# Performance work log

Measured on AMD Instinct MI355X. Metric: run time of the kernel, lower is better.

## Reference

```python
import jax, jax.numpy as jnp
import numpy as np

B, S, D = 4, 1024, 1024
NS = 8            # n_samples
NT = 10           # n_steps
EXP_NOISE = 0.1
STEP = 0.01
TEMP = 1.0
LN_EPS = 1e-5


def _ln(x, g, b):
    m = jnp.mean(x, axis=-1, keepdims=True)
    v = jnp.mean(jnp.square(x - m), axis=-1, keepdims=True)
    return (x - m) * jax.lax.rsqrt(v + LN_EPS) * g + b


def setup_inputs() -> dict:
    key = jax.random.key(0)
    ks = jax.random.split(key, 8)
    sc = 0.02
    return {
        "hidden": jax.random.normal(ks[0], (B, S, D), jnp.float32),
        "W1": jax.random.normal(ks[1], (D, 2 * D), jnp.float32) * sc,
        "b1": jnp.zeros((2 * D,), jnp.float32),
        "ln1_g": jnp.ones((2 * D,), jnp.float32),
        "ln1_b": jnp.zeros((2 * D,), jnp.float32),
        "W2": jax.random.normal(ks[2], (2 * D, D), jnp.float32) * sc,
        "b2": jnp.zeros((D,), jnp.float32),
        "Ew1": jax.random.normal(ks[3], (2 * D, D), jnp.float32) * sc,
        "Eb1": jnp.zeros((D,), jnp.float32),
        "Eln_g": jnp.ones((D,), jnp.float32),
        "Eln_b": jnp.zeros((D,), jnp.float32),
        "Ew2": jax.random.normal(ks[4], (D, D // 2), jnp.float32) * sc,
        "Eb2": jnp.zeros((D // 2,), jnp.float32),
        "Ew3": jax.random.normal(ks[5], (D // 2, 1), jnp.float32) * sc,
        "Eb3": jnp.zeros((1,), jnp.float32),
    }


def reference(hidden, W1, b1, ln1_g, ln1_b, W2, b2,
              Ew1, Eb1, Eln_g, Eln_b, Ew2, Eb2, Ew3, Eb3):
    # context: per-seq mean, identical at every position (keepdim+expand in torch)
    ctx = jnp.mean(hidden, axis=1)                      # [B, D]
    # context_predictor (result is .detach()-ed inside pcn_refine)
    cp = jax.nn.relu(_ln(ctx @ W1 + b1, ln1_g, ln1_b)) @ W2 + b2   # [B, D]
    cp = jax.lax.stop_gradient(cp)

    nkey = jax.random.key(42)
    # n_samples exploration hypotheses: hidden + N(0, exploration_noise)
    expl = jax.random.normal(jax.random.fold_in(nkey, 0), (NS, B, S, D), hidden.dtype)
    hyp = hidden[None] + expl * EXP_NOISE               # [NS, B, S, D]

    cpb = cp[None, :, None, :]                          # broadcast to [NS,B,S,D]

    # PCN refinement: linear pull toward cp + small noise on all but last step
    def step_fn(cur, t):
        cur = cur - STEP * (cur - cpb)
        noise = jax.random.normal(jax.random.fold_in(nkey, t + 1), cur.shape, cur.dtype)
        cur = cur + noise * 0.01 * (t < NT - 1)
        return cur, None

    hyp, _ = jax.lax.scan(step_fn, hyp, jnp.arange(NT))

    # energy_net on concat([latent, context]): split first linear to avoid concat
    Ew1_h, Ew1_c = Ew1[:D], Ew1[D:]
    ce = ctx @ Ew1_c + Eb1                              # context contribution [B, D]
    e = hyp @ Ew1_h + ce[None, :, None, :]              # [NS, B, S, D]
    e = jax.nn.relu(_ln(e, Eln_g, Eln_b))
    e = jax.nn.relu(e @ Ew2 + Eb2)                      # [NS, B, S, D//2]
    e = (e @ Ew3 + Eb3)[..., 0]                         # [NS, B, S]
    energies = jnp.mean(e, axis=2)                      # [NS, B]

    probs = jax.nn.softmax(-energies / TEMP, axis=0)    # [NS, B]
    selected = jnp.einsum('nb,nbsd->bsd', probs, hyp)   # [B, S, D]
    return selected
```

## Files before the change

### kernel.cpp

```cpp
#include <hip/hip_runtime.h>
#include <hip/hip_bf16.h>
#include <stdint.h>
#include <math.h>


#define NS_ 8
#define B_ 4
#define S_ 1024
#define D_ 1024
#define NROWS (NS_*B_*S_)
#define NELEM (1u<<25)

typedef __attribute__((ext_vector_type(8))) short short8;
typedef __attribute__((ext_vector_type(4))) float f32x4;

struct RngParams {
  uint32_t k0[10], k1[10];
  float coef[10];
  float aH, aCP;
};

__host__ __device__ __forceinline__ uint32_t rotl32_(uint32_t x, int r) {
  return (x << r) | (x >> (32 - r));
}

__host__ __device__ __forceinline__ void tf2x32(uint32_t k0, uint32_t k1,
                                                uint32_t x0, uint32_t x1,
                                                uint32_t &o0, uint32_t &o1) {
  uint32_t k2 = k0 ^ k1 ^ 0x1BD11BDAu;
  x0 += k0; x1 += k1;
  x0 += x1; x1 = rotl32_(x1, 13); x1 ^= x0;
  x0 += x1; x1 = rotl32_(x1, 15); x1 ^= x0;
  x0 += x1; x1 = rotl32_(x1, 26); x1 ^= x0;
  x0 += x1; x1 = rotl32_(x1, 6);  x1 ^= x0;
  x0 += k1; x1 += k2 + 1u;
  x0 += x1; x1 = rotl32_(x1, 17); x1 ^= x0;
  x0 += x1; x1 = rotl32_(x1, 29); x1 ^= x0;
  x0 += x1; x1 = rotl32_(x1, 16); x1 ^= x0;
  x0 += x1; x1 = rotl32_(x1, 24); x1 ^= x0;
  x0 += k2; x1 += k0 + 2u;
  x0 += x1; x1 = rotl32_(x1, 13); x1 ^= x0;
  x0 += x1; x1 = rotl32_(x1, 15); x1 ^= x0;
  x0 += x1; x1 = rotl32_(x1, 26); x1 ^= x0;
  x0 += x1; x1 = rotl32_(x1, 6);  x1 ^= x0;
  x0 += k0; x1 += k1 + 3u;
  x0 += x1; x1 = rotl32_(x1, 17); x1 ^= x0;
  x0 += x1; x1 = rotl32_(x1, 29); x1 ^= x0;
  x0 += x1; x1 = rotl32_(x1, 16); x1 ^= x0;
  x0 += x1; x1 = rotl32_(x1, 24); x1 ^= x0;
  x0 += k1; x1 += k2 + 4u;
  x0 += x1; x1 = rotl32_(x1, 13); x1 ^= x0;
  x0 += x1; x1 = rotl32_(x1, 15); x1 ^= x0;
  x0 += x1; x1 = rotl32_(x1, 26); x1 ^= x0;
  x0 += x1; x1 = rotl32_(x1, 6);  x1 ^= x0;
  x0 += k2; x1 += k0 + 5u;
  o0 = x0; o1 = x1;
}

__device__ __forceinline__ float bits_to_normal(uint32_t bits) {
  const float lo = -0.99999994f;
  float f = __uint_as_float((bits >> 9) | 0x3f800000u) - 1.0f;
  float x = fmaxf(lo, f * 2.0f + lo);
  float t = (1.0f - x) * (1.0f + x);
  float w = -__logf(t);
  float p;
  if (w < 5.0f) {
    w = w - 2.5f;
    p = 2.81022636e-08f;
    p = fmaf(p, w, 3.43273939e-07f);
    p = fmaf(p, w, -3.5233877e-06f);
    p = fmaf(p, w, -4.39150654e-06f);
    p = fmaf(p, w, 0.00021858087f);
    p = fmaf(p, w, -0.00125372503f);
    p = fmaf(p, w, -0.00417768164f);
    p = fmaf(p, w, 0.246640727f);
    p = fmaf(p, w, 1.50140941f);
  } else {
    w = sqrtf(w) - 3.0f;
    p = -0.000200214257f;
    p = fmaf(p, w, 0.000100950558f);
    p = fmaf(p, w, 0.00134934322f);
    p = fmaf(p, w, -0.00367342844f);
    p = fmaf(p, w, 0.00573950773f);
    p = fmaf(p, w, -0.0076224613f);
    p = fmaf(p, w, 0.00943887047f);
    p = fmaf(p, w, 1.00167406f);
    p = fmaf(p, w, 2.83297682f);
  }
  return 1.41421356f * (p * x);
}

__device__ __forceinline__ float noise10(const RngParams& P, uint32_t i) {
  float acc = 0.f;
  #pragma unroll
  for (int j = 0; j < 10; ++j) {
    uint32_t w0, w1;
    tf2x32(P.k0[j], P.k1[j], 0u, i, w0, w1);
    acc = fmaf(P.coef[j], bits_to_normal(w0 ^ w1), acc);
  }
  return acc;
}

__device__ __forceinline__ uint16_t bf16u(float x) {
  __hip_bfloat16 h = __float2bfloat16(x);
  return *(uint16_t*)&h;
}
__device__ __forceinline__ float bf2f(uint32_t u) {
  return __uint_as_float(u << 16);
}

__global__ void k_ctxA(const float* __restrict__ hidden, float* __restrict__ part) {
  int b = blockIdx.x >> 6, ch = blockIdx.x & 63;
  const float* p = hidden + (size_t)b * (S_ * D_) + (size_t)ch * 16 * 1024;
  int tid = threadIdx.x;
  #pragma unroll
  for (int k = 0; k < 4; ++k) {
    int d = tid + k * 256;
    float s = 0.f;
    #pragma unroll
    for (int t = 0; t < 16; ++t) s += p[t * 1024 + d];
    part[(size_t)blockIdx.x * 1024 + d] = s;
  }
}
__global__ void k_ctxB(const float* __restrict__ part, float* __restrict__ ctx) {
  int idx = blockIdx.x * 256 + threadIdx.x;
  int b = idx >> 10, d = idx & 1023;
  float s = 0.f;
  #pragma unroll 8
  for (int c = 0; c < 64; ++c) s += part[((size_t)(b * 64 + c)) * 1024 + d];
  ctx[idx] = s * (1.0f / 1024.0f);
}

__global__ void k_fc1(const float* __restrict__ ctx, const float* __restrict__ W1,
                      const float* __restrict__ b1, float* __restrict__ t1) {
  __shared__ float red[4][64];
  int b = blockIdx.x >> 5;
  int j0 = (blockIdx.x & 31) * 64;
  int l = threadIdx.x & 63, w = threadIdx.x >> 6;
  int j = j0 + l;
  const float* c = ctx + b * 1024 + w * 256;
  const float* wp = W1 + (size_t)(w * 256) * 2048 + j;
  float s = 0.f;
  #pragma unroll 8
  for (int k = 0; k < 256; ++k) s += c[k] * wp[(size_t)k * 2048];
  red[w][l] = s; __syncthreads();
  if (w == 0)
    t1[b * 2048 + j] = red[0][l] + red[1][l] + red[2][l] + red[3][l] + b1[j];
}

__global__ void k_ln_relu(float* __restrict__ t1, const float* __restrict__ g,
                          const float* __restrict__ bb) {
  __shared__ float red[256];
  int row = blockIdx.x, tid = threadIdx.x;
  float* x = t1 + row * 2048;
  float v[8];
  #pragma unroll
  for (int q = 0; q < 8; ++q) v[q] = x[tid + q * 256];
  float s = 0.f;
  #pragma unroll
  for (int q = 0; q < 8; ++q) s += v[q];
  red[tid] = s; __syncthreads();
  for (int off = 128; off > 0; off >>= 1) { if (tid < off) red[tid] += red[tid + off]; __syncthreads(); }
  float m = red[0] * (1.0f / 2048.0f);
  __syncthreads();
  float s2 = 0.f;
  #pragma unroll
  for (int q = 0; q < 8; ++q) { float d = v[q] - m; s2 += d * d; }
  red[tid] = s2; __syncthreads();
  for (int off = 128; off > 0; off >>= 1) { if (tid < off) red[tid] += red[tid + off]; __syncthreads(); }
  float var = red[0] * (1.0f / 2048.0f);
  float rs = 1.0f / sqrtf(var + 1e-5f);
  #pragma unroll
  for (int q = 0; q < 8; ++q) {
    int j = tid + q * 256;
    float z = (v[q] - m) * rs * g[j] + bb[j];
    x[j] = fmaxf(z, 0.0f);
  }
}

__global__ void k_fc2(const float* __restrict__ t1, const float* __restrict__ W2,
                      const float* __restrict__ b2, const float* __restrict__ ctx,
                      const float* __restrict__ Ew1c, const float* __restrict__ Eb1,
                      float* __restrict__ cp, float* __restrict__ ce) {
  __shared__ float red[4][64];
  int b = blockIdx.x >> 4;
  int j0 = (blockIdx.x & 15) * 64;
  int l = threadIdx.x & 63, w = threadIdx.x >> 6;
  int j = j0 + l;
  float s = 0.f;
  if (blockIdx.y == 0) {
    const float* a = t1 + b * 2048 + w * 512;
    const float* wp = W2 + (size_t)(w * 512) * 1024 + j;
    #pragma unroll 8
    for (int k = 0; k < 512; ++k) s += a[k] * wp[(size_t)k * 1024];
  } else {
    const float* a = ctx + b * 1024 + w * 256;
    const float* wp = Ew1c + (size_t)(w * 256) * 1024 + j;
    #pragma unroll 8
    for (int k = 0; k < 256; ++k) s += a[k] * wp[(size_t)k * 1024];
  }
  red[w][l] = s; __syncthreads();
  if (w == 0) {
    float r = red[0][l] + red[1][l] + red[2][l] + red[3][l];
    if (blockIdx.y == 0) cp[b * 1024 + j] = r + b2[j];
    else                 ce[b * 1024 + j] = r + Eb1[j];
  }
}

__global__ void k_wcvt(const float* __restrict__ src, uint16_t* __restrict__ dst,
                       int K, int N) {
  __shared__ float tile[64][65];
  int n0 = blockIdx.x * 64, k0 = blockIdx.y * 64;
  int tid = threadIdx.x;
  #pragma unroll
  for (int i = 0; i < 16; ++i) {
    int lin = tid + i * 256;
    int tr = lin >> 6, tc = lin & 63;
    tile[tr][tc] = src[(size_t)(k0 + tr) * N + n0 + tc];
  }
  __syncthreads();
  #pragma unroll
  for (int i = 0; i < 8; ++i) {
    int lin = tid + i * 256;
    int tr = lin >> 5, tc2 = (lin & 31) * 2;
    uint32_t pk = (uint32_t)bf16u(tile[tc2][tr]) | ((uint32_t)bf16u(tile[tc2 + 1][tr]) << 16);
    *(uint32_t*)(&dst[(size_t)(n0 + tr) * K + k0 + tc2]) = pk;
  }
}

#define APAN 0
#define ZPAN 32768
#define BSOF 65536

__device__ __forceinline__ int pswz(int row, int byteInRow) {
  return (row * 2048 + byteInRow) ^ ((row & 7) << 4);
}
__device__ __forceinline__ int bswz(int c, int kbyte) {
  return (c * 64 + kbyte) ^ ((c & 7) << 4);
}

template<bool BIG>
__global__ __launch_bounds__(256, 2) void k_fused(
    const float* __restrict__ hidden, const float* __restrict__ cp,
    const float* __restrict__ ce, uint32_t* __restrict__ hypPairs,
    const uint16_t* __restrict__ WT1, const uint16_t* __restrict__ WT2,
    const float* __restrict__ Eln_g, const float* __restrict__ Eln_b,
    const float* __restrict__ Eb2, const float* __restrict__ Ew3,
    float* __restrict__ erows, RngParams P)
{
  __shared__ __align__(16) char smem[81920];
  const int tid = threadIdx.x;
  const int lane = tid & 63;
  const int w = tid >> 6;
  const int rl = lane & 15;
  const int kg = lane >> 4;
  const int r0 = blockIdx.x * 16;
  const int bidx = (r0 >> 10) & 3;

  for (int q = 0; q < 32; ++q) {
    int p = tid + q * 256;
    int row = p >> 9, cpi = p & 511;
    int c0 = cpi * 2;
    uint32_t i0 = (uint32_t)(r0 + row) * 1024u + (uint32_t)c0;
    float nz0 = noise10(P, i0);
    float nz1 = noise10(P, i0 + 1u);
    uint32_t bsd = i0 & 0x3FFFFFu;
    float2 hv = *(const float2*)(hidden + bsd);
    float2 cv = *(const float2*)(cp + (bidx << 10) + c0);
    float h0 = fmaf(P.aH, hv.x, fmaf(P.aCP, cv.x, nz0));
    float h1 = fmaf(P.aH, hv.y, fmaf(P.aCP, cv.y, nz1));
    uint32_t pk = (uint32_t)bf16u(h0) | ((uint32_t)bf16u(h1) << 16);
    *(uint32_t*)(smem + APAN + pswz(row, c0 * 2)) = pk;
    if (BIG) hypPairs[i0 >> 1] = pk;
  }
  __syncthreads();

  uint4 wreg0, wreg1, wreg2, wreg3;
  for (int g = 0; g < 4; ++g) {
    f32x4 acc[4] = {};
    {
      const uint16_t* srcb = WT1 + (size_t)(g * 256) * 1024;
      int f0 = tid, f1 = tid + 256, f2 = tid + 512, f3 = tid + 768;
      wreg0 = *(const uint4*)(srcb + (size_t)(f0 >> 2) * 1024 + (f0 & 3) * 8);
      wreg1 = *(const uint4*)(srcb + (size_t)(f1 >> 2) * 1024 + (f1 & 3) * 8);
      wreg2 = *(const uint4*)(srcb + (size_t)(f2 >> 2) * 1024 + (f2 & 3) * 8);
      wreg3 = *(const uint4*)(srcb + (size_t)(f3 >> 2) * 1024 + (f3 & 3) * 8);
    }
    for (int kt = 0; kt < 32; ++kt) {
      __syncthreads();
      {
        int f0 = tid, f1 = tid + 256, f2 = tid + 512, f3 = tid + 768;
        *(uint4*)(smem + BSOF + bswz(f0 >> 2, (f0 & 3) * 16)) = wreg0;
        *(uint4*)(smem + BSOF + bswz(f1 >> 2, (f1 & 3) * 16)) = wreg1;
        *(uint4*)(smem + BSOF + bswz(f2 >> 2, (f2 & 3) * 16)) = wreg2;
        *(uint4*)(smem + BSOF + bswz(f3 >> 2, (f3 & 3) * 16)) = wreg3;
      }
      if (kt < 31) {
        const uint16_t* srcb = WT1 + (size_t)(g * 256) * 1024 + (kt + 1) * 32;
        int f0 = tid, f1 = tid + 256, f2 = tid + 512, f3 = tid + 768;
        wreg0 = *(const uint4*)(srcb + (size_t)(f0 >> 2) * 1024 + (f0 & 3) * 8);
        wreg1 = *(const uint4*)(srcb + (size_t)(f1 >> 2) * 1024 + (f1 & 3) * 8);
        wreg2 = *(const uint4*)(srcb + (size_t)(f2 >> 2) * 1024 + (f2 & 3) * 8);
        wreg3 = *(const uint4*)(srcb + (size_t)(f3 >> 2) * 1024 + (f3 & 3) * 8);
      }
      __syncthreads();
      short8 af = *(const short8*)(smem + APAN + pswz(rl, kt * 64 + kg * 16));
      #pragma unroll
      for (int j = 0; j < 4; ++j) {
        int cl = w * 64 + j * 16 + rl;
        short8 bf = *(const short8*)(smem + BSOF + bswz(cl, kg * 16));
        acc[j] = __builtin_amdgcn_mfma_f32_16x16x32_bf16(af, bf, acc[j], 0, 0, 0);
      }
    }
    #pragma unroll
    for (int j = 0; j < 4; ++j) {
      int C = g * 256 + w * 64 + j * 16 + rl;
      float cev = ce[(bidx << 10) + C];
      #pragma unroll
      for (int i = 0; i < 4; ++i) {
        int row = kg * 4 + i;
        *(uint16_t*)(smem + ZPAN + pswz(row, C * 2)) = bf16u(acc[j][i] + cev);
      }
    }
  }
  __syncthreads();

  float* rowm = (float*)(smem + BSOF);
  float* rowr = rowm + 16;
  if (tid < 128) {
    int row = tid >> 3, l8 = tid & 7;
    float s1 = 0.f, s2 = 0.f;
    for (int j = 0; j < 128; ++j) {
      int c = l8 + j * 8;
      float v = bf2f(*(const uint16_t*)(smem + ZPAN + pswz(row, c * 2)));
      s1 += v; s2 = fmaf(v, v, s2);
    }
    #pragma unroll
    for (int o = 4; o > 0; o >>= 1) {
      s1 += __shfl_down(s1, o, 8);
      s2 += __shfl_down(s2, o, 8);
    }
    if (l8 == 0) {
      float m = s1 * (1.0f / 1024.0f);
      float var = fmaxf(s2 * (1.0f / 1024.0f) - m * m, 0.0f);
      rowm[row] = m;
      rowr[row] = 1.0f / sqrtf(var + 1e-5f);
    }
  }
  __syncthreads();

  for (int q = 0; q < 64; ++q) {
    int e = tid + q * 256;
    int row = e >> 10, col = e & 1023;
    uint16_t* zp = (uint16_t*)(smem + ZPAN + pswz(row, col * 2));
    float v = bf2f(*zp);
    float z = (v - rowm[row]) * rowr[row] * Eln_g[col] + Eln_b[col];
    *zp = bf16u(fmaxf(z, 0.f));
  }
  __syncthreads();

  float ep0 = 0.f, ep1 = 0.f, ep2 = 0.f, ep3 = 0.f;
  for (int g = 0; g < 2; ++g) {
    f32x4 acc[4] = {};
    {
      const uint16_t* srcb = WT2 + (size_t)(g * 256) * 1024;
      int f0 = tid, f1 = tid + 256, f2 = tid + 512, f3 = tid + 768;
      wreg0 = *(const uint4*)(srcb + (size_t)(f0 >> 2) * 1024 + (f0 & 3) * 8);
      wreg1 = *(const uint4*)(srcb + (size_t)(f1 >> 2) * 1024 + (f1 & 3) * 8);
      wreg2 = *(const uint4*)(srcb + (size_t)(f2 >> 2) * 1024 + (f2 & 3) * 8);
      wreg3 = *(const uint4*)(srcb + (size_t)(f3 >> 2) * 1024 + (f3 & 3) * 8);
    }
    for (int kt = 0; kt < 32; ++kt) {
      __syncthreads();
      {
        int f0 = tid, f1 = tid + 256, f2 = tid + 512, f3 = tid + 768;
        *(uint4*)(smem + BSOF + bswz(f0 >> 2, (f0 & 3) * 16)) = wreg0;
        *(uint4*)(smem + BSOF + bswz(f1 >> 2, (f1 & 3) * 16)) = wreg1;
        *(uint4*)(smem + BSOF + bswz(f2 >> 2, (f2 & 3) * 16)) = wreg2;
        *(uint4*)(smem + BSOF + bswz(f3 >> 2, (f3 & 3) * 16)) = wreg3;
      }
      if (kt < 31) {
        const uint16_t* srcb = WT2 + (size_t)(g * 256) * 1024 + (kt + 1) * 32;
        int f0 = tid, f1 = tid + 256, f2 = tid + 512, f3 = tid + 768;
        wreg0 = *(const uint4*)(srcb + (size_t)(f0 >> 2) * 1024 + (f0 & 3) * 8);
        wreg1 = *(const uint4*)(srcb + (size_t)(f1 >> 2) * 1024 + (f1 & 3) * 8);
        wreg2 = *(const uint4*)(srcb + (size_t)(f2 >> 2) * 1024 + (f2 & 3) * 8);
        wreg3 = *(const uint4*)(srcb + (size_t)(f3 >> 2) * 1024 + (f3 & 3) * 8);
      }
      __syncthreads();
      short8 af = *(const short8*)(smem + ZPAN + pswz(rl, kt * 64 + kg * 16));
      #pragma unroll
      for (int j = 0; j < 4; ++j) {
        int cl = w * 64 + j * 16 + rl;
        short8 bf = *(const short8*)(smem + BSOF + bswz(cl, kg * 16));
        acc[j] = __builtin_amdgcn_mfma_f32_16x16x32_bf16(af, bf, acc[j], 0, 0, 0);
      }
    }
    #pragma unroll
    for (int j = 0; j < 4; ++j) {
      int C = g * 256 + w * 64 + j * 16 + rl;
      float eb = Eb2[C], w3 = Ew3[C];
      ep0 = fmaf(fmaxf(acc[j][0] + eb, 0.f), w3, ep0);
      ep1 = fmaf(fmaxf(acc[j][1] + eb, 0.f), w3, ep1);
      ep2 = fmaf(fmaxf(acc[j][2] + eb, 0.f), w3, ep2);
      ep3 = fmaf(fmaxf(acc[j][3] + eb, 0.f), w3, ep3);
    }
  }
  #pragma unroll
  for (int m = 1; m < 16; m <<= 1) {
    ep0 += __shfl_xor(ep0, m);
    ep1 += __shfl_xor(ep1, m);
    ep2 += __shfl_xor(ep2, m);
    ep3 += __shfl_xor(ep3, m);
  }
  __syncthreads();
  float* red = (float*)(smem + BSOF + 256);
  if (rl == 0) {
    red[w * 16 + kg * 4 + 0] = ep0;
    red[w * 16 + kg * 4 + 1] = ep1;
    red[w * 16 + kg * 4 + 2] = ep2;
    red[w * 16 + kg * 4 + 3] = ep3;
  }
  __syncthreads();
  if (tid < 16)
    erows[r0 + tid] = red[tid] + red[16 + tid] + red[32 + tid] + red[48 + tid];
}

__global__ void k_energy(const float* __restrict__ erows, const float* __restrict__ Eb3,
                         float* __restrict__ energ) {
  __shared__ float red[256];
  int nb = blockIdx.x, tid = threadIdx.x;
  const float* x = erows + nb * 1024;
  float s = x[tid] + x[tid + 256] + x[tid + 512] + x[tid + 768];
  red[tid] = s; __syncthreads();
  for (int off = 128; off > 0; off >>= 1) { if (tid < off) red[tid] += red[tid + off]; __syncthreads(); }
  if (tid == 0) energ[nb] = red[0] * (1.0f / 1024.0f) + Eb3[0];
}

template<bool BIG>
__global__ __launch_bounds__(256) void k_select(
    const float* __restrict__ hidden, const float* __restrict__ cp,
    const float* __restrict__ energ, const uint32_t* __restrict__ hypPairs,
    float* __restrict__ out, RngParams P)
{
  uint32_t pe = blockIdx.x * 256u + threadIdx.x;
  uint32_t i0 = pe * 2u;
  uint32_t b = (i0 >> 20) & 3u;
  float e[8];
  #pragma unroll
  for (int n = 0; n < 8; ++n) e[n] = -energ[n * 4 + b];
  float mx = e[0];
  #pragma unroll
  for (int n = 1; n < 8; ++n) mx = fmaxf(mx, e[n]);
  float p[8]; float s = 0.f;
  #pragma unroll
  for (int n = 0; n < 8; ++n) { p[n] = expf(e[n] - mx); s += p[n]; }
  float inv = 1.0f / s;
  float a0 = 0.f, a1 = 0.f;
  if (BIG) {
    #pragma unroll
    for (int n = 0; n < 8; ++n) {
      uint32_t pk = hypPairs[pe + ((uint32_t)n << 21)];
      a0 = fmaf(p[n], __uint_as_float(pk << 16), a0);
      a1 = fmaf(p[n], __uint_as_float(pk & 0xffff0000u), a1);
    }
    *(float2*)(out + i0) = make_float2(a0 * inv, a1 * inv);
  } else {
    float2 hv = *(const float2*)(hidden + i0);
    float2 cv = *(const float2*)(cp + ((b << 10) | (i0 & 1023u)));
    #pragma unroll
    for (int n = 0; n < 8; ++n) {
      a0 = fmaf(p[n], noise10(P, i0 + ((uint32_t)n << 22)), a0);
      a1 = fmaf(p[n], noise10(P, i0 + 1u + ((uint32_t)n << 22)), a1);
    }
    float o0 = fmaf(P.aH, hv.x, P.aCP * cv.x) + a0 * inv;
    float o1 = fmaf(P.aH, hv.y, P.aCP * cv.y) + a1 * inv;
    *(float2*)(out + i0) = make_float2(o0, o1);
  }
}

extern "C" void kernel_launch(void* const* d_in, const int* in_sizes, int n_in,
                              void* d_out, int out_size, void* d_ws, size_t ws_size,
                              hipStream_t stream) {
  const float* hidden = (const float*)d_in[0];
  const float* W1    = (const float*)d_in[1];
  const float* b1    = (const float*)d_in[2];
  const float* ln1_g = (const float*)d_in[3];
  const float* ln1_b = (const float*)d_in[4];
  const float* W2    = (const float*)d_in[5];
  const float* b2    = (const float*)d_in[6];
  const float* Ew1   = (const float*)d_in[7];
  const float* Eb1   = (const float*)d_in[8];
  const float* Eln_g = (const float*)d_in[9];
  const float* Eln_b = (const float*)d_in[10];
  const float* Ew2   = (const float*)d_in[11];
  const float* Eb2   = (const float*)d_in[12];
  const float* Ew3   = (const float*)d_in[13];
  const float* Eb3   = (const float*)d_in[14];
  float* out = (float*)d_out;

  const size_t HYP_B  = (size_t)NELEM * 2;
  const size_t WT1_B  = 1024ull * 1024 * 2;
  const size_t WT2_B  = 512ull * 1024 * 2;
  const size_t PART_B = 256ull * 1024 * 4;
  const size_t SMALL_B = (4096 + 8192 + 4096 + 4096 + 32768 + 32) * 4;
  bool big = ws_size >= HYP_B + WT1_B + WT2_B + PART_B + SMALL_B + 1024;

  char* ws = (char*)d_ws;
  uint32_t* hypPairs = nullptr;
  size_t off = 0;
  if (big) { hypPairs = (uint32_t*)ws; off += HYP_B; }
  uint16_t* WT1 = (uint16_t*)(ws + off); off += WT1_B;
  uint16_t* WT2 = (uint16_t*)(ws + off); off += WT2_B;
  float* part  = (float*)(ws + off);     off += PART_B;
  float* ctx   = (float*)(ws + off);
  float* t1    = ctx + 4096;
  float* cp    = t1 + 8192;
  float* ce    = cp + 4096;
  float* erows = ce + 4096;
  float* energ = erows + 32768;

  RngParams P;
  for (uint32_t t = 0; t < 10; ++t) {
    uint32_t o0, o1;
    tf2x32(0u, 42u, 0u, t, o0, o1);
    P.k0[t] = o0; P.k1[t] = o1;
  }
  double a = pow(0.99, 10);
  P.coef[0] = (float)(0.1 * a);
  for (int j = 1; j <= 9; ++j) P.coef[j] = (float)(0.01 * pow(0.99, 10 - j));
  P.aH = (float)a;
  P.aCP = (float)(1.0 - a);

  k_wcvt<<<dim3(16, 16), 256, 0, stream>>>(Ew1, WT1, 1024, 1024);
  k_wcvt<<<dim3(8, 16), 256, 0, stream>>>(Ew2, WT2, 1024, 512);
  k_ctxA<<<256, 256, 0, stream>>>(hidden, part);
  k_ctxB<<<16, 256, 0, stream>>>(part, ctx);
  k_fc1<<<128, 256, 0, stream>>>(ctx, W1, b1, t1);
  k_ln_relu<<<4, 256, 0, stream>>>(t1, ln1_g, ln1_b);
  k_fc2<<<dim3(64, 2), 256, 0, stream>>>(t1, W2, b2, ctx, Ew1 + (size_t)1024 * 1024, Eb1, cp, ce);
  if (big)
    k_fused<true><<<2048, 256, 0, stream>>>(hidden, cp, ce, hypPairs, WT1, WT2,
                                            Eln_g, Eln_b, Eb2, Ew3, erows, P);
  else
    k_fused<false><<<2048, 256, 0, stream>>>(hidden, cp, ce, nullptr, WT1, WT2,
                                             Eln_g, Eln_b, Eb2, Ew3, erows, P);
  k_energy<<<32, 256, 0, stream>>>(erows, Eb3, energ);
  if (big)
    k_select<true><<<8192, 256, 0, stream>>>(hidden, cp, energ, hypPairs, out, P);
  else
    k_select<false><<<8192, 256, 0, stream>>>(hidden, cp, energ, nullptr, out, P);
}
```

Before: 1.166 ms.

## Load weight fragments directly from global memory, dropping LDS staging and barriers

Both in-kernel GEMMs stop staging weight tiles through shared memory with two block barriers per k-step. Each wave now loads its own B-operand fragments straight from global (L2-cached) memory into registers and feeds them to MFMA. The shared buffer shrinks from 80KB to 64KB, which may let more blocks fit per CU. The trade-off is that loads are less coalesced (16-byte pieces spread over rows) and every wave re-fetches the weights from cache, with no cooperative prefetch left to hide latency.

```diff
diff --git a/kernel.cpp b/kernel.cpp
--- a/kernel.cpp
+++ b/kernel.cpp
@@ -230,13 +230,9 @@
 
 #define APAN 0
 #define ZPAN 32768
-#define BSOF 65536
 
 __device__ __forceinline__ int pswz(int row, int byteInRow) {
   return (row * 2048 + byteInRow) ^ ((row & 7) << 4);
-}
-__device__ __forceinline__ int bswz(int c, int kbyte) {
-  return (c * 64 + kbyte) ^ ((c & 7) << 4);
 }
 
 template<bool BIG>
@@ -248,7 +244,8 @@
     const float* __restrict__ Eb2, const float* __restrict__ Ew3,
     float* __restrict__ erows, RngParams P)
 {
-  __shared__ __align__(16) char smem[81920];
+  __shared__ __align__(16) char smem[65536];
+  __shared__ float rowm[16], rowr[16], red[64];
   const int tid = threadIdx.x;
   const int lane = tid & 63;
   const int w = tid >> 6;
@@ -275,42 +272,23 @@
   }
   __syncthreads();
 
-  uint4 wreg0, wreg1, wreg2, wreg3;
   for (int g = 0; g < 4; ++g) {
     f32x4 acc[4] = {};
-    {
-      const uint16_t* srcb = WT1 + (size_t)(g * 256) * 1024;
-      int f0 = tid, f1 = tid + 256, f2 = tid + 512, f3 = tid + 768;
-      wreg0 = *(const uint4*)(srcb + (size_t)(f0 >> 2) * 1024 + (f0 & 3) * 8);
-      wreg1 = *(const uint4*)(srcb + (size_t)(f1 >> 2) * 1024 + (f1 & 3) * 8);
-      wreg2 = *(const uint4*)(srcb + (size_t)(f2 >> 2) * 1024 + (f2 & 3) * 8);
-      wreg3 = *(const uint4*)(srcb + (size_t)(f3 >> 2) * 1024 + (f3 & 3) * 8);
-    }
+    const uint16_t* b0 = WT1 + (size_t)(g * 256 + w * 64 +  0 + rl) * 1024 + kg * 8;
+    const uint16_t* b1p = WT1 + (size_t)(g * 256 + w * 64 + 16 + rl) * 1024 + kg * 8;
+    const uint16_t* b2p = WT1 + (size_t)(g * 256 + w * 64 + 32 + rl) * 1024 + kg * 8;
+    const uint16_t* b3p = WT1 + (size_t)(g * 256 + w * 64 + 48 + rl) * 1024 + kg * 8;
+    #pragma unroll 4
     for (int kt = 0; kt < 32; ++kt) {
-      __syncthreads();
-      {
-        int f0 = tid, f1 = tid + 256, f2 = tid + 512, f3 = tid + 768;
-        *(uint4*)(smem + BSOF + bswz(f0 >> 2, (f0 & 3) * 16)) = wreg0;
-        *(uint4*)(smem + BSOF + bswz(f1 >> 2, (f1 & 3) * 16)) = wreg1;
-        *(uint4*)(smem + BSOF + bswz(f2 >> 2, (f2 & 3) * 16)) = wreg2;
-        *(uint4*)(smem + BSOF + bswz(f3 >> 2, (f3 & 3) * 16)) = wreg3;
-      }
-      if (kt < 31) {
-        const uint16_t* srcb = WT1 + (size_t)(g * 256) * 1024 + (kt + 1) * 32;
-        int f0 = tid, f1 = tid + 256, f2 = tid + 512, f3 = tid + 768;
-        wreg0 = *(const uint4*)(srcb + (size_t)(f0 >> 2) * 1024 + (f0 & 3) * 8);
-        wreg1 = *(const uint4*)(srcb + (size_t)(f1 >> 2) * 1024 + (f1 & 3) * 8);
-        wreg2 = *(const uint4*)(srcb + (size_t)(f2 >> 2) * 1024 + (f2 & 3) * 8);
-        wreg3 = *(const uint4*)(srcb + (size_t)(f3 >> 2) * 1024 + (f3 & 3) * 8);
-      }
-      __syncthreads();
       short8 af = *(const short8*)(smem + APAN + pswz(rl, kt * 64 + kg * 16));
-      #pragma unroll
-      for (int j = 0; j < 4; ++j) {
-        int cl = w * 64 + j * 16 + rl;
-        short8 bf = *(const short8*)(smem + BSOF + bswz(cl, kg * 16));
-        acc[j] = __builtin_amdgcn_mfma_f32_16x16x32_bf16(af, bf, acc[j], 0, 0, 0);
-      }
+      short8 f0 = *(const short8*)(b0  + kt * 32);
+      short8 f1 = *(const short8*)(b1p + kt * 32);
+      short8 f2 = *(const short8*)(b2p + kt * 32);
+      short8 f3 = *(const short8*)(b3p + kt * 32);
+      acc[0] = __builtin_amdgcn_mfma_f32_16x16x32_bf16(af, f0, acc[0], 0, 0, 0);
+      acc[1] = __builtin_amdgcn_mfma_f32_16x16x32_bf16(af, f1, acc[1], 0, 0, 0);
+      acc[2] = __builtin_amdgcn_mfma_f32_16x16x32_bf16(af, f2, acc[2], 0, 0, 0);
+      acc[3] = __builtin_amdgcn_mfma_f32_16x16x32_bf16(af, f3, acc[3], 0, 0, 0);
     }
     #pragma unroll
     for (int j = 0; j < 4; ++j) {
@@ -325,8 +303,6 @@
   }
   __syncthreads();
 
-  float* rowm = (float*)(smem + BSOF);
-  float* rowr = rowm + 16;
   if (tid < 128) {
     int row = tid >> 3, l8 = tid & 7;
     float s1 = 0.f, s2 = 0.f;
@@ -362,39 +338,21 @@
   float ep0 = 0.f, ep1 = 0.f, ep2 = 0.f, ep3 = 0.f;
   for (int g = 0; g < 2; ++g) {
     f32x4 acc[4] = {};
-    {
-      const uint16_t* srcb = WT2 + (size_t)(g * 256) * 1024;
-      int f0 = tid, f1 = tid + 256, f2 = tid + 512, f3 = tid + 768;
-      wreg0 = *(const uint4*)(srcb + (size_t)(f0 >> 2) * 1024 + (f0 & 3) * 8);
-      wreg1 = *(const uint4*)(srcb + (size_t)(f1 >> 2) * 1024 + (f1 & 3) * 8);
-      wreg2 = *(const uint4*)(srcb + (size_t)(f2 >> 2) * 1024 + (f2 & 3) * 8);
-      wreg3 = *(const uint4*)(srcb + (size_t)(f3 >> 2) * 1024 + (f3 & 3) * 8);
-    }
+    const uint16_t* b0 = WT2 + (size_t)(g * 256 + w * 64 +  0 + rl) * 1024 + kg * 8;
+    const uint16_t* b1p = WT2 + (size_t)(g * 256 + w * 64 + 16 + rl) * 1024 + kg * 8;
+    const uint16_t* b2p = WT2 + (size_t)(g * 256 + w * 64 + 32 + rl) * 1024 + kg * 8;
+    const uint16_t* b3p = WT2 + (size_t)(g * 256 + w * 64 + 48 + rl) * 1024 + kg * 8;
+    #pragma unroll 4
     for (int kt = 0; kt < 32; ++kt) {
-      __syncthreads();
-      {
-        int f0 = tid, f1 = tid + 256, f2 = tid + 512, f3 = tid + 768;
-        *(uint4*)(smem + BSOF + bswz(f0 >> 2, (f0 & 3) * 16)) = wreg0;
-        *(uint4*)(smem + BSOF + bswz(f1 >> 2, (f1 & 3) * 16)) = wreg1;
-        *(uint4*)(smem + BSOF + bswz(f2 >> 2, (f2 & 3) * 16)) = wreg2;
-        *(uint4*)(smem + BSOF + bswz(f3 >> 2, (f3 & 3) * 16)) = wreg3;
-      }
-      if (kt < 31) {
-        const uint16_t* srcb = WT2 + (size_t)(g * 256) * 1024 + (kt + 1) * 32;
-        int f0 = tid, f1 = tid + 256, f2 = tid + 512, f3 = tid + 768;
-        wreg0 = *(const uint4*)(srcb + (size_t)(f0 >> 2) * 1024 + (f0 & 3) * 8);
-        wreg1 = *(const uint4*)(srcb + (size_t)(f1 >> 2) * 1024 + (f1 & 3) * 8);
-        wreg2 = *(const uint4*)(srcb + (size_t)(f2 >> 2) * 1024 + (f2 & 3) * 8);
-        wreg3 = *(const uint4*)(srcb + (size_t)(f3 >> 2) * 1024 + (f3 & 3) * 8);
-      }
-      __syncthreads();
       short8 af = *(const short8*)(smem + ZPAN + pswz(rl, kt * 64 + kg * 16));
-      #pragma unroll
-      for (int j = 0; j < 4; ++j) {
-        int cl = w * 64 + j * 16 + rl;
-        short8 bf = *(const short8*)(smem + BSOF + bswz(cl, kg * 16));
-        acc[j] = __builtin_amdgcn_mfma_f32_16x16x32_bf16(af, bf, acc[j], 0, 0, 0);
-      }
+      short8 f0 = *(const short8*)(b0  + kt * 32);
+      short8 f1 = *(const short8*)(b1p + kt * 32);
+      short8 f2 = *(const short8*)(b2p + kt * 32);
+      short8 f3 = *(const short8*)(b3p + kt * 32);
+      acc[0] = __builtin_amdgcn_mfma_f32_16x16x32_bf16(af, f0, acc[0], 0, 0, 0);
+      acc[1] = __builtin_amdgcn_mfma_f32_16x16x32_bf16(af, f1, acc[1], 0, 0, 0);
+      acc[2] = __builtin_amdgcn_mfma_f32_16x16x32_bf16(af, f2, acc[2], 0, 0, 0);
+      acc[3] = __builtin_amdgcn_mfma_f32_16x16x32_bf16(af, f3, acc[3], 0, 0, 0);
     }
     #pragma unroll
     for (int j = 0; j < 4; ++j) {
@@ -413,8 +371,6 @@
     ep2 += __shfl_xor(ep2, m);
     ep3 += __shfl_xor(ep3, m);
   }
-  __syncthreads();
-  float* red = (float*)(smem + BSOF + 256);
   if (rl == 0) {
     red[w * 16 + kg * 4 + 0] = ep0;
     red[w * 16 + kg * 4 + 1] = ep1;
```

After: 1.254 ms. +7.6%, slower.
